# Kernel tuning notes

Hardware: AMD Instinct MI355X
Metric: run time of the kernel (lower is better)

Reference implementation:

```python
import jax, jax.numpy as jnp
import numpy as np
import math

EPS = 1.1920929e-07  # torch default rms_norm eps = finfo(float32).eps

def rms_norm(x):
    return x * jax.lax.rsqrt(jnp.mean(x * x, axis=-1, keepdims=True) + EPS)

def setup_inputs() -> dict:
    key = jax.random.key(0)
    k1, k2, k3, k4 = jax.random.split(key, 4)
    B, T, D = 2, 4096, 2048
    H = 16
    L = (T - 1).bit_length()  # 12
    scale = 0.02
    return {
        "x": jax.random.normal(k1, (B, T, D), dtype=jnp.float32),
        "W_tok": jax.random.normal(k2, (D, D), dtype=jnp.float32) * scale,
        "W_lvl": jax.random.normal(k3, (L * H, D), dtype=jnp.float32) * scale,
        "W_out": jax.random.normal(k4, (D, D), dtype=jnp.float32) * scale,
        "num_heads": H,
    }

def reference(x, W_tok, W_lvl, W_out, num_heads):
    B, T, D = x.shape
    H = num_heads
    Dh = D // H
    L = W_lvl.shape[0] // H  # max_lvls
    inv_sqrt2 = 1.0 / math.sqrt(2.0)

    theta = rms_norm(jnp.einsum('btd,ed->bte', x, W_tok)).reshape(B, T, H, Dh)
    phi = rms_norm(jnp.einsum('btd,ed->bte', x, W_lvl)).reshape(B, T, L, H)

    for l in range(L):  # log-depth butterfly over fixed L levels
        step = 1 << l
        phi_l = phi[:, :, l][..., None]  # [B,T,H,1]
        if step < T:
            theta_prev = jnp.concatenate(
                [jnp.zeros_like(theta[:, :step]), theta[:, :-step]], axis=1)
        else:
            theta_prev = jnp.zeros_like(theta)
        theta = (jnp.cos(phi_l) * theta + jnp.sin(phi_l) * theta_prev) * inv_sqrt2

    y = jnp.einsum('btd,ed->bte', theta.reshape(B, T, D), W_out)
    return y
```

## Files before the change

### kernel.cpp

```cpp
#include <hip/hip_runtime.h>
#include <cstdint>

typedef unsigned short u16;
typedef short bh8 __attribute__((ext_vector_type(8)));
typedef float f32x4 __attribute__((ext_vector_type(4)));

#define EPSF 1.1920929e-07f
#define INV_SQRT2 0.70710678118654752440f

static constexpr size_t OFF_XB   = 0;
static constexpr size_t OFF_WCAT = 33554432;
static constexpr size_t OFF_WOUT = OFF_WCAT + 9437184;
static constexpr size_t OFF_THBF = OFF_WOUT + 8388608;
static constexpr size_t OFF_PHI  = OFF_THBF + 33554432;
static constexpr size_t OFF_TRA  = OFF_PHI + 6291456;
static constexpr size_t OFF_TRB  = OFF_TRA + 6291456;

__device__ __forceinline__ uint32_t f2bf_rne(float f) {
  uint32_t u = __float_as_uint(f);
  u += 0x7fffu + ((u >> 16) & 1u);
  return u >> 16;
}

__device__ __forceinline__ void gload_lds16(const void* g, void* l) {
  __builtin_amdgcn_global_load_lds(
      (const __attribute__((address_space(1))) void*)g,
      (__attribute__((address_space(3))) void*)l, 16, 0, 0);
}

__global__ __launch_bounds__(256)
void cast_f32_bf16(const float* __restrict__ src, u16* __restrict__ dst, int n4) {
  int i = blockIdx.x * blockDim.x + threadIdx.x;
  int stride = gridDim.x * blockDim.x;
  for (; i < n4; i += stride) {
    float4 v = ((const float4*)src)[i];
    uint32_t a = __float_as_uint(v.x); a += 0x7fffu + ((a >> 16) & 1u);
    uint32_t b = __float_as_uint(v.y); b += 0x7fffu + ((b >> 16) & 1u);
    uint32_t c = __float_as_uint(v.z); c += 0x7fffu + ((c >> 16) & 1u);
    uint32_t d = __float_as_uint(v.w); d += 0x7fffu + ((d >> 16) & 1u);
    uint2 o;
    o.x = (a >> 16) | (b & 0xffff0000u);
    o.y = (c >> 16) | (d & 0xffff0000u);
    ((uint2*)dst)[i] = o;
  }
}

__global__ __launch_bounds__(256)
void zero_u16(u16* __restrict__ dst, int n) {
  int i = blockIdx.x * blockDim.x + threadIdx.x;
  int stride = gridDim.x * blockDim.x;
  for (; i < n; i += stride) dst[i] = 0;
}

template<int SPLIT>
__global__ __launch_bounds__(256)
void gemm_bt(const u16* __restrict__ A, const u16* __restrict__ B,
             float* __restrict__ C0, float* __restrict__ C1,
             int K, int ntiles) {
  __shared__ u16 As[128 * 64];
  __shared__ u16 Bs[128 * 64];
  const int tid  = threadIdx.x;
  const int w    = tid >> 6;
  const int lane = tid & 63;
  const int mt = blockIdx.x / ntiles, nt = blockIdx.x % ntiles;
  const int wm = (w >> 1) << 6, wn = (w & 1) << 6;
  const int Kb = K * 2;

  const char* Ab = (const char*)(A + (size_t)mt * 128 * K);
  const char* Bb = (const char*)(B + (size_t)nt * 128 * K);
  char* AsB = (char*)As;
  char* BsB = (char*)Bs;

  const int srow  = w * 8 + (lane >> 3);
  const int scolb = (lane & 7) << 4;

  f32x4 acc[4][4] = {};

  for (int kt = 0; kt < K; kt += 64) {
    #pragma unroll
    for (int i = 0; i < 4; ++i) {
      int row = i * 32 + srow;
      int src = scolb ^ ((row & 7) << 4);
      gload_lds16(Ab + (size_t)row * Kb + kt * 2 + src, AsB + i * 4096 + w * 1024);
      gload_lds16(Bb + (size_t)row * Kb + kt * 2 + src, BsB + i * 4096 + w * 1024);
    }
    __syncthreads();
    #pragma unroll
    for (int kk = 0; kk < 2; ++kk) {
      const int kbyte = kk * 64 + ((lane >> 4) << 4);
      bh8 af[4], bfr[4];
      #pragma unroll
      for (int m = 0; m < 4; ++m) {
        int ar = wm + m * 16 + (lane & 15);
        af[m] = *(const bh8*)(AsB + ar * 128 + (kbyte ^ ((ar & 7) << 4)));
        int br = wn + m * 16 + (lane & 15);
        bfr[m] = *(const bh8*)(BsB + br * 128 + (kbyte ^ ((br & 7) << 4)));
      }
      #pragma unroll
      for (int m = 0; m < 4; ++m)
        #pragma unroll
        for (int n = 0; n < 4; ++n)
          acc[m][n] = __builtin_amdgcn_mfma_f32_16x16x32_bf16(af[m], bfr[n], acc[m][n], 0, 0, 0);
    }
    __syncthreads();
  }

  const int crow0 = mt * 128 + wm + ((lane >> 4) << 2);
  const int ccol0 = nt * 128 + wn + (lane & 15);
  #pragma unroll
  for (int m = 0; m < 4; ++m) {
    #pragma unroll
    for (int n = 0; n < 4; ++n) {
      int gn = ccol0 + n * 16;
      #pragma unroll
      for (int r = 0; r < 4; ++r) {
        int gm = crow0 + m * 16 + r;
        if (SPLIT) {
          if (gn < 2048)      C0[(size_t)gm * 2048 + gn] = acc[m][n][r];
          else if (gn < 2240) C1[(size_t)gm * 192 + (gn - 2048)] = acc[m][n][r];
        } else {
          C0[(size_t)gm * 2048 + gn] = acc[m][n][r];
        }
      }
    }
  }
}

__global__ __launch_bounds__(256)
void rmsnorm_rows(float* __restrict__ th) {
  const int row = blockIdx.x;
  const int tid = threadIdx.x;
  float* p = th + (size_t)row * 2048;
  float4 a = ((const float4*)p)[tid];
  float4 b = ((const float4*)p)[tid + 256];
  float ss = a.x*a.x + a.y*a.y + a.z*a.z + a.w*a.w
           + b.x*b.x + b.y*b.y + b.z*b.z + b.w*b.w;
  #pragma unroll
  for (int o = 32; o > 0; o >>= 1) ss += __shfl_down(ss, o);
  __shared__ float red[4];
  if ((tid & 63) == 0) red[tid >> 6] = ss;
  __syncthreads();
  float tot = red[0] + red[1] + red[2] + red[3];
  float s = rsqrtf(tot * (1.0f / 2048.0f) + EPSF);
  a.x *= s; a.y *= s; a.z *= s; a.w *= s;
  b.x *= s; b.y *= s; b.z *= s; b.w *= s;
  ((float4*)p)[tid] = a;
  ((float4*)p)[tid + 256] = b;
}

__global__ __launch_bounds__(64)
void phi_pass(const float* __restrict__ phiraw,
              float* __restrict__ trigA, float* __restrict__ trigB) {
  const int row = blockIdx.x;
  const int tid = threadIdx.x;
  const float* pr = phiraw + (size_t)row * 192;
  float v0 = pr[tid], v1 = pr[tid + 64], v2 = pr[tid + 128];
  float ss = v0 * v0 + v1 * v1 + v2 * v2;
  #pragma unroll
  for (int o = 32; o > 0; o >>= 1) ss += __shfl_down(ss, o);
  ss = __shfl(ss, 0);
  const float sc = rsqrtf(ss * (1.0f / 192.0f) + EPSF);
  const int b = row >> 12, t = row & 4095;
  const int q = t >> 6, r = t & 63;
  float v[3] = {v0, v1, v2};
  #pragma unroll
  for (int j = 0; j < 3; ++j) {
    int e = j * 64 + tid;
    int l = e >> 4, h = e & 15;
    float ph = v[j] * sc;
    float sn, cs;
    sincosf(ph, &sn, &cs);
    if (l < 6) {
      size_t idx = ((size_t)((b * 16 + h) * 6 + l)) * 4096 + t;
      trigA[idx] = cs; trigA[idx + 786432] = sn;
    } else {
      size_t idx = ((size_t)((b * 16 + h) * 6 + (l - 6))) * 4096 + (size_t)(r * 64 + q);
      trigB[idx] = cs; trigB[idx + 786432] = sn;
    }
  }
}

__global__ __launch_bounds__(512)
void butterflyA(const float* __restrict__ in, u16* __restrict__ outb,
                const float* __restrict__ trigA) {
  __shared__ float L[512 * 32];
  const int tc = blockIdx.x, ec = blockIdx.y, b = blockIdx.z;
  const int tid = threadIdx.x;
  const int t0 = tc * 449;
  const int e0 = ec * 32;
  const int h = e0 >> 7;
  const int pr = tid >> 3;
  const int c4 = (tid & 7) << 2;

  #pragma unroll
  for (int s = 0; s < 8; ++s) {
    int p = pr + s * 64;
    int t = t0 - 63 + p;
    float4 v = make_float4(0.f, 0.f, 0.f, 0.f);
    if (t >= 0 && t < 4096)
      v = *(const float4*)&in[((size_t)(b * 4096 + t)) * 2048 + e0 + c4];
    *(float4*)&L[p * 32 + c4] = v;
  }
  __syncthreads();

  for (int l = 0; l < 6; ++l) {
    const int step = 1 << l;
    const float* cosT = trigA + ((size_t)((b * 16 + h) * 6 + l)) * 4096;
    const float* sinT = cosT + 786432;
    float4 nv[8];
    #pragma unroll
    for (int s = 0; s < 8; ++s) {
      int p = pr + s * 64;
      int t = t0 - 63 + p;
      float4 cur = *(const float4*)&L[p * 32 + c4];
      float4 prev = make_float4(0.f, 0.f, 0.f, 0.f);
      if (p >= step) prev = *(const float4*)&L[(p - step) * 32 + c4];
      float cs = 0.f, sn = 0.f;
      if (t >= 0 && t < 4096) { cs = cosT[t]; sn = sinT[t]; }
      nv[s].x = (cs * cur.x + sn * prev.x) * INV_SQRT2;
      nv[s].y = (cs * cur.y + sn * prev.y) * INV_SQRT2;
      nv[s].z = (cs * cur.z + sn * prev.z) * INV_SQRT2;
      nv[s].w = (cs * cur.w + sn * prev.w) * INV_SQRT2;
    }
    __syncthreads();
    #pragma unroll
    for (int s = 0; s < 8; ++s) {
      int p = pr + s * 64;
      *(float4*)&L[p * 32 + c4] = nv[s];
    }
    __syncthreads();
  }

  #pragma unroll
  for (int s = 0; s < 8; ++s) {
    int p = pr + s * 64;
    int t = t0 - 63 + p;
    if (p >= 63 && t < 4096) {
      float4 v = *(const float4*)&L[p * 32 + c4];
      uint32_t a = f2bf_rne(v.x), bb = f2bf_rne(v.y), c = f2bf_rne(v.z), d = f2bf_rne(v.w);
      uint2 o;
      o.x = a | (bb << 16);
      o.y = c | (d << 16);
      *(uint2*)&outb[((size_t)(b * 4096 + t)) * 2048 + e0 + c4] = o;
    }
  }
}

__global__ __launch_bounds__(256)
void butterflyB(const u16* __restrict__ in, u16* __restrict__ outb,
                const float* __restrict__ trigB) {
  __shared__ float L[64 * 128];
  const int r = blockIdx.x, h = blockIdx.y, b = blockIdx.z;
  const int tid = threadIdx.x;
  const int qr = tid >> 5;
  const int d4 = (tid & 31) << 2;

  #pragma unroll
  for (int s = 0; s < 8; ++s) {
    int q = qr + s * 8;
    int t = q * 64 + r;
    uint2 o = *(const uint2*)&in[((size_t)(b * 4096 + t)) * 2048 + h * 128 + d4];
    float4 v;
    v.x = __uint_as_float((o.x & 0xffffu) << 16);
    v.y = __uint_as_float(o.x & 0xffff0000u);
    v.z = __uint_as_float((o.y & 0xffffu) << 16);
    v.w = __uint_as_float(o.y & 0xffff0000u);
    *(float4*)&L[q * 128 + d4] = v;
  }
  __syncthreads();

  for (int l = 0; l < 6; ++l) {
    const int qs = 1 << l;
    const float* cosT = trigB + ((size_t)((b * 16 + h) * 6 + l)) * 4096 + r * 64;
    const float* sinT = cosT + 786432;
    float4 nv[8];
    #pragma unroll
    for (int s = 0; s < 8; ++s) {
      int q = qr + s * 8;
      float4 cur = *(const float4*)&L[q * 128 + d4];
      float4 prev = make_float4(0.f, 0.f, 0.f, 0.f);
      if (q >= qs) prev = *(const float4*)&L[(q - qs) * 128 + d4];
      float cs = cosT[q], sn = sinT[q];
      nv[s].x = (cs * cur.x + sn * prev.x) * INV_SQRT2;
      nv[s].y = (cs * cur.y + sn * prev.y) * INV_SQRT2;
      nv[s].z = (cs * cur.z + sn * prev.z) * INV_SQRT2;
      nv[s].w = (cs * cur.w + sn * prev.w) * INV_SQRT2;
    }
    __syncthreads();
    #pragma unroll
    for (int s = 0; s < 8; ++s) {
      int q = qr + s * 8;
      *(float4*)&L[q * 128 + d4] = nv[s];
    }
    __syncthreads();
  }

  #pragma unroll
  for (int s = 0; s < 8; ++s) {
    int q = qr + s * 8;
    int t = q * 64 + r;
    float4 v = *(const float4*)&L[q * 128 + d4];
    uint32_t a = f2bf_rne(v.x), bb = f2bf_rne(v.y), c = f2bf_rne(v.z), d = f2bf_rne(v.w);
    uint2 o;
    o.x = a | (bb << 16);
    o.y = c | (d << 16);
    *(uint2*)&outb[((size_t)(b * 4096 + t)) * 2048 + h * 128 + d4] = o;
  }
}

extern "C" void kernel_launch(void* const* d_in, const int* in_sizes, int n_in,
                              void* d_out, int out_size, void* d_ws, size_t ws_size,
                              hipStream_t stream) {
  const float* x    = (const float*)d_in[0];
  const float* Wtok = (const float*)d_in[1];
  const float* Wlvl = (const float*)d_in[2];
  const float* Wout = (const float*)d_in[3];

  char* ws = (char*)d_ws;
  u16*   xb     = (u16*)(ws + OFF_XB);
  u16*   wcat   = (u16*)(ws + OFF_WCAT);
  u16*   woutb  = (u16*)(ws + OFF_WOUT);
  u16*   thbfA  = (u16*)(ws + OFF_XB);
  u16*   thbfB  = (u16*)(ws + OFF_THBF);
  float* phiraw = (float*)(ws + OFF_PHI);
  float* trigA  = (float*)(ws + OFF_TRA);
  float* trigB  = (float*)(ws + OFF_TRB);
  float* out    = (float*)d_out;

  cast_f32_bf16<<<2048, 256, 0, stream>>>(x, xb, 4194304);
  cast_f32_bf16<<<1024, 256, 0, stream>>>(Wtok, wcat, 1048576);
  cast_f32_bf16<<<384, 256, 0, stream>>>(Wlvl, wcat + (size_t)2048 * 2048, 98304);
  zero_u16<<<128, 256, 0, stream>>>(wcat + (size_t)2240 * 2048, 131072);
  cast_f32_bf16<<<1024, 256, 0, stream>>>(Wout, woutb, 1048576);

  gemm_bt<1><<<64 * 18, 256, 0, stream>>>(xb, wcat, out, phiraw, 2048, 18);

  rmsnorm_rows<<<8192, 256, 0, stream>>>(out);

  phi_pass<<<8192, 64, 0, stream>>>(phiraw, trigA, trigB);

  butterflyA<<<dim3(10, 64, 2), 512, 0, stream>>>(out, thbfA, trigA);

  butterflyB<<<dim3(64, 16, 2), 256, 0, stream>>>(thbfA, thbfB, trigB);

  gemm_bt<0><<<64 * 16, 256, 0, stream>>>(thbfB, woutb, out, nullptr, 2048, 16);
}
```

Measured before the change: 461.9 us.

## Replace GEMM with 256x128 triple-buffered pipelined kernel and defer rmsnorm scaling

Swaps the simple single-buffered 128x128 GEMM for a 512-thread, 256x128-tile kernel. It uses a three-stage LDS ring fed by direct global-to-LDS loads, split barriers with s_setprio around the MFMA blocks, and an XCD-aware remapping of workgroup indices. The rmsnorm kernel now only computes per-row scales, and butterflyA applies them as it loads, which removes a full read-modify-write pass over the theta buffer. In exchange the GEMM hardcodes K=2048 and the LDS layout, and a new fragment layout must match the bf16 inputs, which makes it fragile.

```diff
diff --git a/kernel.cpp b/kernel.cpp
--- a/kernel.cpp
+++ b/kernel.cpp
@@ -10,6 +10,7 @@
 
 static constexpr size_t OFF_XB   = 0;
 static constexpr size_t OFF_WCAT = 33554432;
+static constexpr size_t OFF_SC   = OFF_WCAT + 9175040;
 static constexpr size_t OFF_WOUT = OFF_WCAT + 9437184;
 static constexpr size_t OFF_THBF = OFF_WOUT + 8388608;
 static constexpr size_t OFF_PHI  = OFF_THBF + 33554432;
@@ -53,59 +54,97 @@
 }
 
 template<int SPLIT>
-__global__ __launch_bounds__(256)
-void gemm_bt(const u16* __restrict__ A, const u16* __restrict__ B,
+__global__ __launch_bounds__(512, 2)
+void gemm_dp(const u16* __restrict__ A, const u16* __restrict__ B,
              float* __restrict__ C0, float* __restrict__ C1,
-             int K, int ntiles) {
-  __shared__ u16 As[128 * 64];
-  __shared__ u16 Bs[128 * 64];
+             int ntiles, int nwg) {
+  __shared__ __align__(16) char ldsb[73728];
   const int tid  = threadIdx.x;
   const int w    = tid >> 6;
   const int lane = tid & 63;
-  const int mt = blockIdx.x / ntiles, nt = blockIdx.x % ntiles;
-  const int wm = (w >> 1) << 6, wn = (w & 1) << 6;
-  const int Kb = K * 2;
-
-  const char* Ab = (const char*)(A + (size_t)mt * 128 * K);
-  const char* Bb = (const char*)(B + (size_t)nt * 128 * K);
-  char* AsB = (char*)As;
-  char* BsB = (char*)Bs;
-
-  const int srow  = w * 8 + (lane >> 3);
-  const int scolb = (lane & 7) << 4;
+  const int cpx = nwg >> 3;
+  const int wg  = (blockIdx.x & 7) * cpx + (blockIdx.x >> 3);
+  const int mt = wg / ntiles, nt = wg % ntiles;
+  const int wm = (w >> 1) << 6;
+  const int wn = (w & 1) << 6;
+  const int wmR = (w >> 1) << 2;
+  const int wnR = (w & 1) << 2;
+  const size_t Kb = 4096;
+
+  const char* Ab = (const char*)A + (size_t)mt * 256 * Kb;
+  const char* Bb = (const char*)B + (size_t)nt * 128 * Kb;
+
+  const int sA1 = 512 + tid;
+  const int rA0 = ((tid >> 6) << 4) + (tid & 15);
+  const int gA0 = ((tid >> 4) & 3) << 4;
+  const int rA1 = ((sA1 >> 6) << 4) + (sA1 & 15);
+  const int gA1 = ((sA1 >> 4) & 3) << 4;
+  const char* srcA0 = Ab + (size_t)rA0 * Kb + gA0;
+  const char* srcA1 = Ab + (size_t)rA1 * Kb + gA1;
+  const char* srcB  = Bb + (size_t)rA0 * Kb + gA0;
+  const int wB = w * 1024;
+  const int lo = ((lane >> 4) << 8) + ((lane & 15) << 4);
 
   f32x4 acc[4][4] = {};
 
-  for (int kt = 0; kt < K; kt += 64) {
-    #pragma unroll
-    for (int i = 0; i < 4; ++i) {
-      int row = i * 32 + srow;
-      int src = scolb ^ ((row & 7) << 4);
-      gload_lds16(Ab + (size_t)row * Kb + kt * 2 + src, AsB + i * 4096 + w * 1024);
-      gload_lds16(Bb + (size_t)row * Kb + kt * 2 + src, BsB + i * 4096 + w * 1024);
-    }
-    __syncthreads();
-    #pragma unroll
-    for (int kk = 0; kk < 2; ++kk) {
-      const int kbyte = kk * 64 + ((lane >> 4) << 4);
-      bh8 af[4], bfr[4];
-      #pragma unroll
-      for (int m = 0; m < 4; ++m) {
-        int ar = wm + m * 16 + (lane & 15);
-        af[m] = *(const bh8*)(AsB + ar * 128 + (kbyte ^ ((ar & 7) << 4)));
-        int br = wn + m * 16 + (lane & 15);
-        bfr[m] = *(const bh8*)(BsB + br * 128 + (kbyte ^ ((br & 7) << 4)));
-      }
-      #pragma unroll
-      for (int m = 0; m < 4; ++m)
-        #pragma unroll
-        for (int n = 0; n < 4; ++n)
-          acc[m][n] = __builtin_amdgcn_mfma_f32_16x16x32_bf16(af[m], bfr[n], acc[m][n], 0, 0, 0);
-    }
-    __syncthreads();
-  }
-
-  const int crow0 = mt * 128 + wm + ((lane >> 4) << 2);
+#define STAGE_A(tt, cc) do { \
+    gload_lds16(srcA0 + (tt) * 64, ldsb + (cc) * 16384 + wB); \
+    gload_lds16(srcA1 + (tt) * 64, ldsb + (cc) * 16384 + 8192 + wB); } while (0)
+#define STAGE_B(tt, cc) \
+    gload_lds16(srcB + (tt) * 64, ldsb + 49152 + (cc) * 8192 + wB)
+
+  STAGE_A(0, 0); STAGE_B(0, 0);
+  STAGE_A(1, 1); STAGE_B(1, 1);
+  asm volatile("s_waitcnt vmcnt(3)" ::: "memory");
+  __builtin_amdgcn_s_barrier();
+
+  int c = 0;
+  for (int t = 0; t < 64; ++t) {
+    int c2 = c + 2; if (c2 >= 3) c2 -= 3;
+    const char* Abase = ldsb + c * 16384;
+    const char* Bbase = ldsb + 49152 + c * 8192;
+    if (t < 62) STAGE_A(t + 2, c2);
+    bh8 a0 = *(const bh8*)(Abase + (wmR + 0) * 1024 + lo);
+    bh8 a1 = *(const bh8*)(Abase + (wmR + 1) * 1024 + lo);
+    bh8 b0 = *(const bh8*)(Bbase + (wnR + 0) * 1024 + lo);
+    bh8 b1 = *(const bh8*)(Bbase + (wnR + 1) * 1024 + lo);
+    bh8 b2 = *(const bh8*)(Bbase + (wnR + 2) * 1024 + lo);
+    bh8 b3 = *(const bh8*)(Bbase + (wnR + 3) * 1024 + lo);
+    __builtin_amdgcn_s_barrier();
+    __builtin_amdgcn_s_setprio(1);
+    acc[0][0] = __builtin_amdgcn_mfma_f32_16x16x32_bf16(a0, b0, acc[0][0], 0, 0, 0);
+    acc[0][1] = __builtin_amdgcn_mfma_f32_16x16x32_bf16(a0, b1, acc[0][1], 0, 0, 0);
+    acc[0][2] = __builtin_amdgcn_mfma_f32_16x16x32_bf16(a0, b2, acc[0][2], 0, 0, 0);
+    acc[0][3] = __builtin_amdgcn_mfma_f32_16x16x32_bf16(a0, b3, acc[0][3], 0, 0, 0);
+    acc[1][0] = __builtin_amdgcn_mfma_f32_16x16x32_bf16(a1, b0, acc[1][0], 0, 0, 0);
+    acc[1][1] = __builtin_amdgcn_mfma_f32_16x16x32_bf16(a1, b1, acc[1][1], 0, 0, 0);
+    acc[1][2] = __builtin_amdgcn_mfma_f32_16x16x32_bf16(a1, b2, acc[1][2], 0, 0, 0);
+    acc[1][3] = __builtin_amdgcn_mfma_f32_16x16x32_bf16(a1, b3, acc[1][3], 0, 0, 0);
+    __builtin_amdgcn_s_setprio(0);
+    __builtin_amdgcn_s_barrier();
+    if (t < 62) STAGE_B(t + 2, c2);
+    bh8 a2 = *(const bh8*)(Abase + (wmR + 2) * 1024 + lo);
+    bh8 a3 = *(const bh8*)(Abase + (wmR + 3) * 1024 + lo);
+    __builtin_amdgcn_s_barrier();
+    __builtin_amdgcn_s_setprio(1);
+    acc[2][0] = __builtin_amdgcn_mfma_f32_16x16x32_bf16(a2, b0, acc[2][0], 0, 0, 0);
+    acc[2][1] = __builtin_amdgcn_mfma_f32_16x16x32_bf16(a2, b1, acc[2][1], 0, 0, 0);
+    acc[2][2] = __builtin_amdgcn_mfma_f32_16x16x32_bf16(a2, b2, acc[2][2], 0, 0, 0);
+    acc[2][3] = __builtin_amdgcn_mfma_f32_16x16x32_bf16(a2, b3, acc[2][3], 0, 0, 0);
+    acc[3][0] = __builtin_amdgcn_mfma_f32_16x16x32_bf16(a3, b0, acc[3][0], 0, 0, 0);
+    acc[3][1] = __builtin_amdgcn_mfma_f32_16x16x32_bf16(a3, b1, acc[3][1], 0, 0, 0);
+    acc[3][2] = __builtin_amdgcn_mfma_f32_16x16x32_bf16(a3, b2, acc[3][2], 0, 0, 0);
+    acc[3][3] = __builtin_amdgcn_mfma_f32_16x16x32_bf16(a3, b3, acc[3][3], 0, 0, 0);
+    __builtin_amdgcn_s_setprio(0);
+    if (t < 62) asm volatile("s_waitcnt vmcnt(3)" ::: "memory");
+    else        asm volatile("s_waitcnt vmcnt(0)" ::: "memory");
+    __builtin_amdgcn_s_barrier();
+    c = (c == 2) ? 0 : c + 1;
+  }
+#undef STAGE_A
+#undef STAGE_B
+
+  const int crow0 = mt * 256 + wm + ((lane >> 4) << 2);
   const int ccol0 = nt * 128 + wn + (lane & 15);
   #pragma unroll
   for (int m = 0; m < 4; ++m) {
@@ -127,10 +166,10 @@
 }
 
 __global__ __launch_bounds__(256)
-void rmsnorm_rows(float* __restrict__ th) {
+void rmsnorm_scales(const float* __restrict__ th, float* __restrict__ sc) {
   const int row = blockIdx.x;
   const int tid = threadIdx.x;
-  float* p = th + (size_t)row * 2048;
+  const float* p = th + (size_t)row * 2048;
   float4 a = ((const float4*)p)[tid];
   float4 b = ((const float4*)p)[tid + 256];
   float ss = a.x*a.x + a.y*a.y + a.z*a.z + a.w*a.w
@@ -140,12 +179,10 @@
   __shared__ float red[4];
   if ((tid & 63) == 0) red[tid >> 6] = ss;
   __syncthreads();
-  float tot = red[0] + red[1] + red[2] + red[3];
-  float s = rsqrtf(tot * (1.0f / 2048.0f) + EPSF);
-  a.x *= s; a.y *= s; a.z *= s; a.w *= s;
-  b.x *= s; b.y *= s; b.z *= s; b.w *= s;
-  ((float4*)p)[tid] = a;
-  ((float4*)p)[tid + 256] = b;
+  if (tid == 0) {
+    float tot = red[0] + red[1] + red[2] + red[3];
+    sc[row] = rsqrtf(tot * (1.0f / 2048.0f) + EPSF);
+  }
 }
 
 __global__ __launch_bounds__(64)
@@ -182,7 +219,7 @@
 
 __global__ __launch_bounds__(512)
 void butterflyA(const float* __restrict__ in, u16* __restrict__ outb,
-                const float* __restrict__ trigA) {
+                const float* __restrict__ trigA, const float* __restrict__ scales) {
   __shared__ float L[512 * 32];
   const int tc = blockIdx.x, ec = blockIdx.y, b = blockIdx.z;
   const int tid = threadIdx.x;
@@ -197,8 +234,11 @@
     int p = pr + s * 64;
     int t = t0 - 63 + p;
     float4 v = make_float4(0.f, 0.f, 0.f, 0.f);
-    if (t >= 0 && t < 4096)
+    if (t >= 0 && t < 4096) {
       v = *(const float4*)&in[((size_t)(b * 4096 + t)) * 2048 + e0 + c4];
+      float scl = scales[b * 4096 + t];
+      v.x *= scl; v.y *= scl; v.z *= scl; v.w *= scl;
+    }
     *(float4*)&L[p * 32 + c4] = v;
   }
   __syncthreads();
@@ -322,6 +362,7 @@
   u16*   woutb  = (u16*)(ws + OFF_WOUT);
   u16*   thbfA  = (u16*)(ws + OFF_XB);
   u16*   thbfB  = (u16*)(ws + OFF_THBF);
+  float* scales = (float*)(ws + OFF_SC);
   float* phiraw = (float*)(ws + OFF_PHI);
   float* trigA  = (float*)(ws + OFF_TRA);
   float* trigB  = (float*)(ws + OFF_TRB);
@@ -333,15 +374,15 @@
   zero_u16<<<128, 256, 0, stream>>>(wcat + (size_t)2240 * 2048, 131072);
   cast_f32_bf16<<<1024, 256, 0, stream>>>(Wout, woutb, 1048576);
 
-  gemm_bt<1><<<64 * 18, 256, 0, stream>>>(xb, wcat, out, phiraw, 2048, 18);
-
-  rmsnorm_rows<<<8192, 256, 0, stream>>>(out);
+  gemm_dp<1><<<576, 512, 0, stream>>>(xb, wcat, out, phiraw, 18, 576);
+
+  rmsnorm_scales<<<8192, 256, 0, stream>>>(out, scales);
 
   phi_pass<<<8192, 64, 0, stream>>>(phiraw, trigA, trigB);
 
-  butterflyA<<<dim3(10, 64, 2), 512, 0, stream>>>(out, thbfA, trigA);
+  butterflyA<<<dim3(10, 64, 2), 512, 0, stream>>>(out, thbfA, trigA, scales);
 
   butterflyB<<<dim3(64, 16, 2), 256, 0, stream>>>(thbfA, thbfB, trigB);
 
-  gemm_bt<0><<<64 * 16, 256, 0, stream>>>(thbfB, woutb, out, nullptr, 2048, 16);
-}
+  gemm_dp<0><<<512, 512, 0, stream>>>(thbfB, woutb, out, nullptr, 16, 512);
+}
```

New measurement: 481.3 us. 1.04x slower.
